# Kernel optimization log

Hardware: AMD Instinct MI355X
Metric: run time of the kernel (lower is better)

## Reference

```python
import jax, jax.numpy as jnp
import numpy as np

K = 16            # neighbors per node
NB = 8            # number_of_basis
MAX_RADIUS = 10.0
MUL_1E = 32       # multiplicity of the 1e output block
DIM_0E = 64       # 64x0e block (structurally zero: no 1o x 0e -> 0e path)
DIM_2E = 80       # 16x2e block (structurally zero: no 1o x 0e -> 2e path)


def knn_edges(coords):
    """coords [B,N,3] -> (senders, receivers) flat int32 indices of length B*N*K.
    Edge (j -> i): j is one of the K nearest neighbors of i (self excluded),
    matching torch_geometric knn_graph(loop=False, flow=source_to_target)."""
    B, N, _ = coords.shape
    n2 = jnp.sum(coords * coords, -1)                       # [B,N]
    d2 = n2[:, :, None] + n2[:, None, :] - 2.0 * jnp.einsum('bnd,bmd->bnm', coords, coords)
    d2 = d2 + jnp.eye(N, dtype=coords.dtype) * 1e10         # exclude self-loops
    _, idx = jax.lax.top_k(-d2, K)                          # [B,N,K] neighbor ids per node
    offs = (jnp.arange(B) * N)[:, None, None]
    senders = (idx + offs).reshape(-1)
    receivers = (jnp.broadcast_to(jnp.arange(N)[None, :, None], (B, N, K)) + offs).reshape(-1)
    return senders, receivers


def gaussian_soft_one_hot(x, number):
    # x in [0,1], shape [E,1] -> [E,number]
    centers = jnp.linspace(0.0, 1.0, number).astype(x.dtype)
    sigma = 1.0 / number
    g = jnp.exp(-(x - centers) ** 2 / (2.0 * sigma * sigma))
    s = jnp.sum(g, -1, keepdims=True)
    s = jnp.where(s > 0, s, jnp.ones_like(s))
    return g / s


def setup_inputs():
    key = jax.random.key(0)
    ks = jax.random.split(key, 6)
    B, N = 8, 4096
    coords = jax.random.normal(ks[0], (B, N, 3), dtype=jnp.float32) * 10.0
    atom_types = jax.random.randint(ks[1], (B, N), 0, 20)
    residue_types = jax.random.randint(ks[2], (B, N), 0, 21)
    tp_weight = jax.random.normal(ks[3], (NB, MUL_1E), dtype=jnp.float32) / np.sqrt(NB)
    atom_emb = jax.random.normal(ks[4], (20, 112), dtype=jnp.float32).at[0].set(0.0)   # padding_idx=0
    res_emb = jax.random.normal(ks[5], (21, 112), dtype=jnp.float32).at[0].set(0.0)    # padding_idx=0
    return {"coords": coords, "atom_types": atom_types, "residue_types": residue_types,
            "tp_weight": tp_weight, "atom_emb": atom_emb, "res_emb": res_emb}


def reference(coords, atom_types, residue_types, tp_weight, atom_emb, res_emb):
    B, N, _ = coords.shape
    E = B * N * K
    senders, receivers = knn_edges(coords)
    cf = coords.reshape(-1, 3)
    r = cf[senders] - cf[receivers]                           # [E,3]
    dist = jnp.linalg.norm(r, axis=-1, keepdims=True)         # [E,1]
    r_hat = r / (dist + 1e-8)
    cutoff = jnp.clip(dist / MAX_RADIUS, 0.0, 1.0)
    rb = gaussian_soft_one_hot(cutoff, NB)                    # [E,NB]
    # FullyConnectedTensorProduct(1x1o/1e, NBx0e -> ... 32x1e ...):
    feat_1e = jnp.einsum('ev,vw,em->ewm', rb, tp_weight, r_hat) / np.sqrt(3.0)  # [E,32,3]
    # scatter_mean over receivers
    num = jax.ops.segment_sum(feat_1e.reshape(E, MUL_1E * 3), receivers, num_segments=B * N)
    cnt = jax.ops.segment_sum(jnp.ones((E,), coords.dtype), receivers, num_segments=B * N)
    agg_1e = (num / jnp.maximum(cnt, 1.0)[:, None]).reshape(B, N, MUL_1E * 3)
    zeros0 = jnp.zeros((B, N, DIM_0E), coords.dtype)
    zeros2 = jnp.zeros((B, N, DIM_2E), coords.dtype)
    pos_feats = jnp.concatenate([zeros0, agg_1e, zeros2], -1)  # [B,N,240]
    node_features = jnp.concatenate([pos_feats, atom_emb[atom_types], res_emb[residue_types]], -1)
    return node_features  # [B,N,464]
```

## Files before the change

### kernel.cpp

```cpp
#include <hip/hip_runtime.h>
#include <hip/hip_bf16.h>

#define NN    4096
#define KNEI  16
#define QPW   4
#define WPB   16
#define BLOCK (WPB * 64)
#define QPB   (WPB * QPW)
#define NEGB  -3.0e38f
#define PACKM 0xFFFFFFC0

typedef float f32x2 __attribute__((ext_vector_type(2)));

__device__ __forceinline__ int rlane(int v, int l)
{ return __builtin_amdgcn_readlane(v, l); }
__device__ __forceinline__ float rlanef(float v, int l)
{ return __int_as_float(__builtin_amdgcn_readlane(__float_as_int(v), l)); }

template<int CTRL>
__device__ __forceinline__ void amax_step(float& f, int& i)
{
    int fs = __builtin_amdgcn_update_dpp(__float_as_int(f), __float_as_int(f),
                                         CTRL, 0xF, 0xF, false);
    int is = __builtin_amdgcn_update_dpp(i, i, CTRL, 0xF, 0xF, false);
    float ff = __int_as_float(fs);
    bool gt = ff > f;
    f = gt ? ff : f;
    i = gt ? is : i;
}

__device__ __forceinline__ void wave_amax(float f, int i, float& M, int& mi)
{
    amax_step<0x111>(f, i); amax_step<0x112>(f, i); amax_step<0x114>(f, i);
    amax_step<0x118>(f, i); amax_step<0x142>(f, i); amax_step<0x143>(f, i);
    M  = rlanef(f, 63);
    mi = rlane(i, 63);
}

__device__ __forceinline__ void row_amax(float& f, int& i)
{
    amax_step<0x121>(f, i); amax_step<0x122>(f, i);
    amax_step<0x124>(f, i); amax_step<0x128>(f, i);
}

__device__ __forceinline__ float row16_sum_dpp(float v)
{
    float f = v;
#define STEPA(CTRL)                                                          \
    { int s_ = __builtin_amdgcn_update_dpp(0, __float_as_int(f),             \
               (CTRL), 0xF, 0xF, true);                                      \
      f += __int_as_float(s_); }
    STEPA(0x111) STEPA(0x112) STEPA(0x114) STEPA(0x118)
#undef STEPA
    return f;
}

__device__ __forceinline__ float bpermf(int abyte, float v)
{ return __int_as_float(__builtin_amdgcn_ds_bpermute(abyte, __float_as_int(v))); }

__device__ __forceinline__ float sel4f(float a, float b, float c, float d, int q)
{
    float lo = (q & 1) ? b : a;
    float hi = (q & 1) ? d : c;
    return (q & 2) ? hi : lo;
}

#define LADDER(dp, b, s)                                          \
    {  (s) = __builtin_amdgcn_fmed3f((dp), (s), (b));             \
       (b) = fmaxf((b), (dp)); }

#define SELFFIX(q, b, s)                                                     \
    {  int cb_ = __float_as_int(b) & 63;                                     \
       if ((((cb_) << 6) | (lane ^ cb_)) == q0 + (q)) { (b) = (s); (s) = NEGB; } \
       int cs_ = __float_as_int(s) & 63;                                     \
       if ((((cs_) << 6) | (lane ^ cs_)) == q0 + (q)) { (s) = NEGB; } }

#define REPLAY(q, xq, yq, zq)                                                \
    {   int colq = rlane(colw, 16 * (q));                                    \
        int kq   = rlane(kw,   16 * (q));                                    \
        int j2 = (lane << 6) | (colq ^ lane);                                \
        float4 P = pts[j2];                                                  \
        float scr = fmaf(P.x, (xq), fmaf(P.y, (yq), fmaf(P.z, (zq), P.w)));  \
        float sf = __int_as_float((__float_as_int(scr) & PACKM) | lane);     \
        if (j2 == q0 + (q)) sf = NEGB;                                       \
        _Pragma("unroll")                                                    \
        for (int t = 0; t < KNEI; ++t) {                                     \
            int sv = rlane(selIdx, 16 * (q) + t);                            \
            if (j2 == sv) sf = NEGB;                                         \
        }                                                                    \
        float M1; int i1;                                                    \
        wave_amax(sf, j2, M1, i1);                                           \
        float sf2 = (j2 == i1) ? NEGB : sf;                                  \
        float M2; int i2;                                                    \
        wave_amax(sf2, j2, M2, i2);                                          \
        bool ow = (lane == 16 * (q) + (colq & 15));                          \
        if (kq == 0)      { pb0 = ow ? M1 : pb0; ps0 = ow ? M2 : ps0; }      \
        else if (kq == 1) { pb1 = ow ? M1 : pb1; ps1 = ow ? M2 : ps1; }      \
        else if (kq == 2) { pb2 = ow ? M1 : pb2; ps2 = ow ? M2 : ps2; }      \
        else              { pb3 = ow ? M1 : pb3; ps3 = ow ? M2 : ps3; }      \
    }

#define PROMOTE(k, pb, ps)                                                   \
    {   bool pk = own && (kw == (k));                                        \
        exh = exh || (pk && ((ps) == NEGB));                                 \
        (pb) = pk ? (ps)  : (pb);                                            \
        (ps) = pk ? NEGB : (ps);                                             \
    }

__global__ __launch_bounds__(BLOCK, 8)
void protein_enc_kernel(const float* __restrict__ coords,
                        const int*   __restrict__ atypes,
                        const int*   __restrict__ rtypes,
                        const float* __restrict__ tpw,
                        const float* __restrict__ aemb,
                        const float* __restrict__ remb,
                        float* __restrict__ out)
{
    __shared__ float4 pts[NN];
    __shared__ float  sW[8 * 32];

    const int tid  = threadIdx.x;
    const int lane = tid & 63;
    const int wv   = tid >> 6;
    const int bpb  = NN / QPB;
    const int batch    = blockIdx.x / bpb;
    const int nodeBase = (blockIdx.x % bpb) * QPB;

    const float* cb = coords + (size_t)batch * NN * 3;

    for (int p = tid; p < NN; p += BLOCK) {
        float x = cb[3*p], y = cb[3*p+1], z = cb[3*p+2];
        pts[p] = make_float4(x, y, z, -0.5f * (x*x + y*y + z*z));
    }
    if (tid < 256) sW[tid] = tpw[tid];
    __syncthreads();

    const int q0 = nodeBase + wv * QPW;
    const float4 P0 = pts[q0],   P1 = pts[q0+1];
    const float4 P2 = pts[q0+2], P3 = pts[q0+3];
    const float x0 = P0.x, y0 = P0.y, z0 = P0.z;
    const float x1 = P1.x, y1 = P1.y, z1 = P1.z;
    const float x2 = P2.x, y2 = P2.y, z2 = P2.z;
    const float x3 = P3.x, y3 = P3.y, z3 = P3.z;

    const f32x2 qAx = {x0, x1}, qAy = {y0, y1}, qAz = {z0, z1};
    const f32x2 qBx = {x2, x3}, qBy = {y2, y3}, qBz = {z2, z3};

    float b0 = NEGB, s0 = NEGB, b1 = NEGB, s1 = NEGB;
    float b2 = NEGB, s2 = NEGB, b3 = NEGB, s3 = NEGB;

    #pragma unroll 8
    for (int c = 0; c < NN / 64; ++c) {
        int j = (c << 6) | (lane ^ c);
        float4 P = pts[j];
        f32x2 Px = {P.x, P.x}, Py = {P.y, P.y}, Pz = {P.z, P.z}, Pw = {P.w, P.w};
        f32x2 dA = __builtin_elementwise_fma(Px, qAx,
                   __builtin_elementwise_fma(Py, qAy,
                   __builtin_elementwise_fma(Pz, qAz, Pw)));
        f32x2 dB = __builtin_elementwise_fma(Px, qBx,
                   __builtin_elementwise_fma(Py, qBy,
                   __builtin_elementwise_fma(Pz, qBz, Pw)));
        float d0 = __int_as_float((__float_as_int(dA.x) & PACKM) | c);
        float d1 = __int_as_float((__float_as_int(dA.y) & PACKM) | c);
        float d2 = __int_as_float((__float_as_int(dB.x) & PACKM) | c);
        float d3 = __int_as_float((__float_as_int(dB.y) & PACKM) | c);
        LADDER(d0, b0, s0)
        LADDER(d1, b1, s1)
        LADDER(d2, b2, s2)
        LADDER(d3, b3, s3)
    }

    SELFFIX(0, b0, s0)
    SELFFIX(1, b1, s1)
    SELFFIX(2, b2, s2)
    SELFFIX(3, b3, s3)

    const int q  = lane >> 4;
    const int gt = lane & 15;
    float pb0, pb1, pb2, pb3, ps0, ps1, ps2, ps3;
    {
        const int ab = gt << 2;
#define PULL(K, PB, PS)                                                      \
        {   int a = ab + ((K) << 6);                                         \
            PB = sel4f(bpermf(a,b0), bpermf(a,b1), bpermf(a,b2), bpermf(a,b3), q); \
            PS = sel4f(bpermf(a,s0), bpermf(a,s1), bpermf(a,s2), bpermf(a,s3), q); \
        }
        PULL(0, pb0, ps0)
        PULL(1, pb1, ps1)
        PULL(2, pb2, ps2)
        PULL(3, pb3, ps3)
#undef PULL
    }

    int selIdx = -1;

    #pragma unroll 1
    for (int r = 0; r < KNEI; ++r) {
        float f = fmaxf(fmaxf(pb0, pb1), fmaxf(pb2, pb3));
        int k = (f == pb3) ? 3 : ((f == pb2) ? 2 : ((f == pb1) ? 1 : 0));
        int cw = __float_as_int(f) & 63;
        int col = gt + (k << 4);
        int jl = (cw << 6) | (col ^ cw);
        int i = (k << 12) | jl;
        row_amax(f, i);

        int j  = i & 4095;
        int kw = i >> 12;
        int colw = (j & 63) ^ (j >> 6);
        bool own = (gt == (colw & 15));

        if (gt == r) selIdx = j;

        bool exh = false;
        PROMOTE(0, pb0, ps0)
        PROMOTE(1, pb1, ps1)
        PROMOTE(2, pb2, ps2)
        PROMOTE(3, pb3, ps3)

        unsigned long long ex = __ballot(exh);
        if (ex) {
            if ((ex >>  0) & 0xFFFFull) REPLAY(0, x0, y0, z0)
            if ((ex >> 16) & 0xFFFFull) REPLAY(1, x1, y1, z1)
            if ((ex >> 32) & 0xFFFFull) REPLAY(2, x2, y2, z2)
            if ((ex >> 48) & 0xFFFFull) REPLAY(3, x3, y3, z3)
        }
    }

    float xq = (q & 2) ? ((q & 1) ? x3 : x2) : ((q & 1) ? x1 : x0);
    float yq = (q & 2) ? ((q & 1) ? y3 : y2) : ((q & 1) ? y1 : y0);
    float zq = (q & 2) ? ((q & 1) ? z3 : z2) : ((q & 1) ? z1 : z0);

    float4 P = pts[selIdx];
    float rx = P.x - xq, ry = P.y - yq, rz = P.z - zq;
    float dist = sqrtf(rx*rx + ry*ry + rz*rz);
    float inv  = 1.0f / (dist + 1e-8f);
    float hx = rx * inv, hy = ry * inv, hz = rz * inv;
    float cu = fminf(dist / 10.0f, 1.0f);
    float gg[8], ssum = 0.0f;
    #pragma unroll
    for (int v = 0; v < 8; ++v) {
        float d = cu - (float)v * (1.0f / 7.0f);
        gg[v] = expf(d * d * -32.0f);
        ssum += gg[v];
    }
    float is = 1.0f / ssum;
    float S[24];
    #pragma unroll
    for (int v = 0; v < 8; ++v) {
        float rbv = gg[v] * is;
        S[3*v]   = rbv * hx;
        S[3*v+1] = rbv * hy;
        S[3*v+2] = rbv * hz;
    }
    #pragma unroll
    for (int t = 0; t < 24; ++t) S[t] = row16_sum_dpp(S[t]);

    float wcol[8];
    #pragma unroll
    for (int v = 0; v < 8; ++v) wcol[v] = sW[32*v + (lane & 31)];

    const float scale = 0.036084391824351613f;
    const float4 z4 = make_float4(0.f, 0.f, 0.f, 0.f);

    #pragma unroll
    for (int qq = 0; qq < QPW; ++qq) {
        const int gq = batch * NN + q0 + qq;
        float sg[24];
        #pragma unroll
        for (int t = 0; t < 24; ++t) sg[t] = rlanef(S[t], 16 * qq + 15);

        float* onode = out + (size_t)gq * 464;
        float4* o4 = (float4*)onode;
        if (lane < 16)       o4[lane] = z4;
        else if (lane < 36)  o4[lane + 24] = z4;

        if (lane < 32) {
            float a0 = 0.f, a1 = 0.f, a2 = 0.f;
            #pragma unroll
            for (int v = 0; v < 8; ++v) {
                a0 = fmaf(wcol[v], sg[3*v],   a0);
                a1 = fmaf(wcol[v], sg[3*v+1], a1);
                a2 = fmaf(wcol[v], sg[3*v+2], a2);
            }
            onode[64 + 3*lane]     = a0 * scale;
            onode[64 + 3*lane + 1] = a1 * scale;
            onode[64 + 3*lane + 2] = a2 * scale;
        }

        const int at = atypes[gq];
        const int rt = rtypes[gq];
        if (lane < 56) {
            float4 v = (lane < 28)
                ? ((const float4*)(aemb + 112*at))[lane]
                : ((const float4*)(remb + 112*rt))[lane - 28];
            o4[60 + lane] = v;
        }
    }
}

extern "C" void kernel_launch(void* const* d_in, const int* in_sizes, int n_in,
                              void* d_out, int out_size, void* d_ws, size_t ws_size,
                              hipStream_t stream)
{
    const float* coords = (const float*)d_in[0];
    const int*   at     = (const int*)  d_in[1];
    const int*   rt     = (const int*)  d_in[2];
    const float* tpw    = (const float*)d_in[3];
    const float* ae     = (const float*)d_in[4];
    const float* re     = (const float*)d_in[5];
    float* out = (float*)d_out;

    const int B = in_sizes[1] / NN;
    dim3 grid(B * (NN / QPB));
    protein_enc_kernel<<<grid, BLOCK, 0, stream>>>(coords, at, rt, tpw, ae, re, out);
}
```

Baseline: 73.80 us.

## Vectorize top-2 ladder, simplify k-select round, factor Gaussian exps

The main scan's top-2 ladder now runs on packed f32x2 vectors with max/min instead of per-query fmed3. The 16-round selection replaces the row argmax that carried indices with a float-only DPP max, followed by a ballot to pick the winning lane. Selected indices go to shared memory, so replay reads them with int4 loads instead of 16 readlanes. The 8 Gaussian basis exps become 2 exps plus a multiplicative recurrence with precomputed constants, which may cost some accuracy or risk underflow in the small terms.

```diff
diff --git a/kernel.cpp b/kernel.cpp
--- a/kernel.cpp
+++ b/kernel.cpp
@@ -11,11 +11,20 @@
 #define PACKM 0xFFFFFFC0
 
 typedef float f32x2 __attribute__((ext_vector_type(2)));
+typedef int   i32x2 __attribute__((ext_vector_type(2)));
 
 __device__ __forceinline__ int rlane(int v, int l)
 { return __builtin_amdgcn_readlane(v, l); }
 __device__ __forceinline__ float rlanef(float v, int l)
 { return __int_as_float(__builtin_amdgcn_readlane(__float_as_int(v), l)); }
+
+template<int CTRL>
+__device__ __forceinline__ float rmax_step(float f)
+{
+    int s_ = __builtin_amdgcn_update_dpp(__float_as_int(f), __float_as_int(f),
+                                         CTRL, 0xF, 0xF, false);
+    return fmaxf(f, __int_as_float(s_));
+}
 
 template<int CTRL>
 __device__ __forceinline__ void amax_step(float& f, int& i)
@@ -35,12 +44,6 @@
     amax_step<0x118>(f, i); amax_step<0x142>(f, i); amax_step<0x143>(f, i);
     M  = rlanef(f, 63);
     mi = rlane(i, 63);
-}
-
-__device__ __forceinline__ void row_amax(float& f, int& i)
-{
-    amax_step<0x121>(f, i); amax_step<0x122>(f, i);
-    amax_step<0x124>(f, i); amax_step<0x128>(f, i);
 }
 
 __device__ __forceinline__ float row16_sum_dpp(float v)
@@ -65,46 +68,37 @@
     return (q & 2) ? hi : lo;
 }
 
-#define LADDER(dp, b, s)                                          \
-    {  (s) = __builtin_amdgcn_fmed3f((dp), (s), (b));             \
-       (b) = fmaxf((b), (dp)); }
-
 #define SELFFIX(q, b, s)                                                     \
     {  int cb_ = __float_as_int(b) & 63;                                     \
        if ((((cb_) << 6) | (lane ^ cb_)) == q0 + (q)) { (b) = (s); (s) = NEGB; } \
        int cs_ = __float_as_int(s) & 63;                                     \
        if ((((cs_) << 6) | (lane ^ cs_)) == q0 + (q)) { (s) = NEGB; } }
 
-#define REPLAY(q, xq, yq, zq)                                                \
-    {   int colq = rlane(colw, 16 * (q));                                    \
-        int kq   = rlane(kw,   16 * (q));                                    \
+#define REPLAY(qq, xq, yq, zq)                                               \
+    {   int wq = __ffsll(ex & (0xFFFFull << ((qq) * 16))) - 1;               \
+        int colq = rlane(col, wq);                                           \
+        int kq   = rlane(kf,  wq);                                           \
         int j2 = (lane << 6) | (colq ^ lane);                                \
-        float4 P = pts[j2];                                                  \
-        float scr = fmaf(P.x, (xq), fmaf(P.y, (yq), fmaf(P.z, (zq), P.w)));  \
+        float4 Pp = pts[j2];                                                 \
+        float scr = fmaf(Pp.x,(xq), fmaf(Pp.y,(yq), fmaf(Pp.z,(zq), Pp.w))); \
         float sf = __int_as_float((__float_as_int(scr) & PACKM) | lane);     \
-        if (j2 == q0 + (q)) sf = NEGB;                                       \
-        _Pragma("unroll")                                                    \
-        for (int t = 0; t < KNEI; ++t) {                                     \
-            int sv = rlane(selIdx, 16 * (q) + t);                            \
-            if (j2 == sv) sf = NEGB;                                         \
-        }                                                                    \
+        if (j2 == q0 + (qq)) sf = NEGB;                                      \
+        const int4* sp = (const int4*)&sel[wv * 64 + ((qq) << 4)];           \
+        int4 sa = sp[0], sb = sp[1], sc = sp[2], sd = sp[3];                 \
+        if (j2==sa.x || j2==sa.y || j2==sa.z || j2==sa.w) sf = NEGB;         \
+        if (j2==sb.x || j2==sb.y || j2==sb.z || j2==sb.w) sf = NEGB;         \
+        if (j2==sc.x || j2==sc.y || j2==sc.z || j2==sc.w) sf = NEGB;         \
+        if (j2==sd.x || j2==sd.y || j2==sd.z || j2==sd.w) sf = NEGB;         \
         float M1; int i1;                                                    \
         wave_amax(sf, j2, M1, i1);                                           \
         float sf2 = (j2 == i1) ? NEGB : sf;                                  \
         float M2; int i2;                                                    \
         wave_amax(sf2, j2, M2, i2);                                          \
-        bool ow = (lane == 16 * (q) + (colq & 15));                          \
+        bool ow = (lane == (qq) * 16 + (colq & 15));                         \
         if (kq == 0)      { pb0 = ow ? M1 : pb0; ps0 = ow ? M2 : ps0; }      \
         else if (kq == 1) { pb1 = ow ? M1 : pb1; ps1 = ow ? M2 : ps1; }      \
         else if (kq == 2) { pb2 = ow ? M1 : pb2; ps2 = ow ? M2 : ps2; }      \
         else              { pb3 = ow ? M1 : pb3; ps3 = ow ? M2 : ps3; }      \
-    }
-
-#define PROMOTE(k, pb, ps)                                                   \
-    {   bool pk = own && (kw == (k));                                        \
-        exh = exh || (pk && ((ps) == NEGB));                                 \
-        (pb) = pk ? (ps)  : (pb);                                            \
-        (ps) = pk ? NEGB : (ps);                                             \
     }
 
 __global__ __launch_bounds__(BLOCK, 8)
@@ -118,6 +112,7 @@
 {
     __shared__ float4 pts[NN];
     __shared__ float  sW[8 * 32];
+    __shared__ int    sel[WPB * 64];
 
     const int tid  = threadIdx.x;
     const int lane = tid & 63;
@@ -133,6 +128,7 @@
         pts[p] = make_float4(x, y, z, -0.5f * (x*x + y*y + z*z));
     }
     if (tid < 256) sW[tid] = tpw[tid];
+    sel[wv * 64 + lane] = -1;
     __syncthreads();
 
     const int q0 = nodeBase + wv * QPW;
@@ -145,30 +141,35 @@
 
     const f32x2 qAx = {x0, x1}, qAy = {y0, y1}, qAz = {z0, z1};
     const f32x2 qBx = {x2, x3}, qBy = {y2, y3}, qBz = {z2, z3};
-
-    float b0 = NEGB, s0 = NEGB, b1 = NEGB, s1 = NEGB;
-    float b2 = NEGB, s2 = NEGB, b3 = NEGB, s3 = NEGB;
+    const i32x2 M2v = {(int)PACKM, (int)PACKM};
+
+    f32x2 bA = {NEGB, NEGB}, sA = {NEGB, NEGB};
+    f32x2 bB = {NEGB, NEGB}, sB = {NEGB, NEGB};
 
     #pragma unroll 8
     for (int c = 0; c < NN / 64; ++c) {
         int j = (c << 6) | (lane ^ c);
         float4 P = pts[j];
-        f32x2 Px = {P.x, P.x}, Py = {P.y, P.y}, Pz = {P.z, P.z}, Pw = {P.w, P.w};
-        f32x2 dA = __builtin_elementwise_fma(Px, qAx,
-                   __builtin_elementwise_fma(Py, qAy,
-                   __builtin_elementwise_fma(Pz, qAz, Pw)));
-        f32x2 dB = __builtin_elementwise_fma(Px, qBx,
-                   __builtin_elementwise_fma(Py, qBy,
-                   __builtin_elementwise_fma(Pz, qBz, Pw)));
-        float d0 = __int_as_float((__float_as_int(dA.x) & PACKM) | c);
-        float d1 = __int_as_float((__float_as_int(dA.y) & PACKM) | c);
-        float d2 = __int_as_float((__float_as_int(dB.x) & PACKM) | c);
-        float d3 = __int_as_float((__float_as_int(dB.y) & PACKM) | c);
-        LADDER(d0, b0, s0)
-        LADDER(d1, b1, s1)
-        LADDER(d2, b2, s2)
-        LADDER(d3, b3, s3)
-    }
+        f32x2 vx = {P.x, P.x}, vy = {P.y, P.y}, vz = {P.z, P.z}, vw = {P.w, P.w};
+        f32x2 dA = __builtin_elementwise_fma(vx, qAx,
+                   __builtin_elementwise_fma(vy, qAy,
+                   __builtin_elementwise_fma(vz, qAz, vw)));
+        f32x2 dB = __builtin_elementwise_fma(vx, qBx,
+                   __builtin_elementwise_fma(vy, qBy,
+                   __builtin_elementwise_fma(vz, qBz, vw)));
+        i32x2 cc = {c, c};
+        f32x2 pA = __builtin_bit_cast(f32x2,
+                     (__builtin_bit_cast(i32x2, dA) & M2v) | cc);
+        f32x2 pB = __builtin_bit_cast(f32x2,
+                     (__builtin_bit_cast(i32x2, dB) & M2v) | cc);
+        sA = __builtin_elementwise_max(sA, __builtin_elementwise_min(pA, bA));
+        bA = __builtin_elementwise_max(bA, pA);
+        sB = __builtin_elementwise_max(sB, __builtin_elementwise_min(pB, bB));
+        bB = __builtin_elementwise_max(bB, pB);
+    }
+
+    float b0 = bA.x, b1 = bA.y, b2 = bB.x, b3 = bB.y;
+    float s0 = sA.x, s1 = sA.y, s2 = sB.x, s3 = sB.y;
 
     SELFFIX(0, b0, s0)
     SELFFIX(1, b1, s1)
@@ -192,32 +193,34 @@
 #undef PULL
     }
 
-    int selIdx = -1;
+    const unsigned long long gmask = 0xFFFFull << (q << 4);
+    const int selbase = wv * 64 + (q << 4);
 
     #pragma unroll 1
     for (int r = 0; r < KNEI; ++r) {
         float f = fmaxf(fmaxf(pb0, pb1), fmaxf(pb2, pb3));
-        int k = (f == pb3) ? 3 : ((f == pb2) ? 2 : ((f == pb1) ? 1 : 0));
-        int cw = __float_as_int(f) & 63;
-        int col = gt + (k << 4);
-        int jl = (cw << 6) | (col ^ cw);
-        int i = (k << 12) | jl;
-        row_amax(f, i);
-
-        int j  = i & 4095;
-        int kw = i >> 12;
-        int colw = (j & 63) ^ (j >> 6);
-        bool own = (gt == (colw & 15));
-
-        if (gt == r) selIdx = j;
-
-        bool exh = false;
-        PROMOTE(0, pb0, ps0)
-        PROMOTE(1, pb1, ps1)
-        PROMOTE(2, pb2, ps2)
-        PROMOTE(3, pb3, ps3)
-
-        unsigned long long ex = __ballot(exh);
+        f = rmax_step<0x121>(f); f = rmax_step<0x122>(f);
+        f = rmax_step<0x124>(f); f = rmax_step<0x128>(f);
+        bool c0 = (pb0 == f), c1 = (pb1 == f), c2 = (pb2 == f), c3 = (pb3 == f);
+        unsigned long long m = __ballot(c0 | c1 | c2 | c3);
+        int w = __ffsll(m & gmask) - 1;
+        bool iwin = (lane == w);
+        int kf = c0 ? 0 : (c1 ? 1 : (c2 ? 2 : 3));
+        bool o0 = iwin && c0;
+        bool o1 = iwin && !c0 && c1;
+        bool o2 = iwin && !c0 && !c1 && c2;
+        bool o3 = iwin && !c0 && !c1 && !c2;
+        int cw  = __float_as_int(f) & 63;
+        int col = gt + (kf << 4);
+        int jw  = (cw << 6) | (col ^ cw);
+        if (iwin) sel[selbase + r] = jw;
+        float pskf = o1 ? ps1 : (o2 ? ps2 : (o3 ? ps3 : ps0));
+        bool e = iwin && (pskf == NEGB);
+        pb0 = o0 ? ps0 : pb0;  ps0 = o0 ? NEGB : ps0;
+        pb1 = o1 ? ps1 : pb1;  ps1 = o1 ? NEGB : ps1;
+        pb2 = o2 ? ps2 : pb2;  ps2 = o2 ? NEGB : ps2;
+        pb3 = o3 ? ps3 : pb3;  ps3 = o3 ? NEGB : ps3;
+        unsigned long long ex = __ballot(e);
         if (ex) {
             if ((ex >>  0) & 0xFFFFull) REPLAY(0, x0, y0, z0)
             if ((ex >> 16) & 0xFFFFull) REPLAY(1, x1, y1, z1)
@@ -226,6 +229,8 @@
         }
     }
 
+    int selIdx = sel[wv * 64 + lane];
+
     float xq = (q & 2) ? ((q & 1) ? x3 : x2) : ((q & 1) ? x1 : x0);
     float yq = (q & 2) ? ((q & 1) ? y3 : y2) : ((q & 1) ? y1 : y0);
     float zq = (q & 2) ? ((q & 1) ? z3 : z2) : ((q & 1) ? z1 : z0);
@@ -236,13 +241,16 @@
     float inv  = 1.0f / (dist + 1e-8f);
     float hx = rx * inv, hy = ry * inv, hz = rz * inv;
     float cu = fminf(dist / 10.0f, 1.0f);
-    float gg[8], ssum = 0.0f;
-    #pragma unroll
-    for (int v = 0; v < 8; ++v) {
-        float d = cu - (float)v * (1.0f / 7.0f);
-        gg[v] = expf(d * d * -32.0f);
-        ssum += gg[v];
-    }
+    float A = expf(cu * cu * -32.0f);
+    float E = expf(cu * (64.0f / 7.0f));
+    const float K[8] = {1.0f, 0.5204501f, 0.0733697f, 0.00280164f,
+                        2.897772e-05f, 8.11857e-08f, 6.16130e-11f,
+                        1.2664166e-14f};
+    float gg[8];
+    float t = A, ssum = A;
+    gg[0] = A;
+    #pragma unroll
+    for (int v = 1; v < 8; ++v) { t *= E; gg[v] = t * K[v]; ssum += gg[v]; }
     float is = 1.0f / ssum;
     float S[24];
     #pragma unroll
@@ -253,7 +261,7 @@
         S[3*v+2] = rbv * hz;
     }
     #pragma unroll
-    for (int t = 0; t < 24; ++t) S[t] = row16_sum_dpp(S[t]);
+    for (int t2 = 0; t2 < 24; ++t2) S[t2] = row16_sum_dpp(S[t2]);
 
     float wcol[8];
     #pragma unroll
@@ -267,7 +275,7 @@
         const int gq = batch * NN + q0 + qq;
         float sg[24];
         #pragma unroll
-        for (int t = 0; t < 24; ++t) sg[t] = rlanef(S[t], 16 * qq + 15);
+        for (int t2 = 0; t2 < 24; ++t2) sg[t2] = rlanef(S[t2], 16 * qq + 15);
 
         float* onode = out + (size_t)gq * 464;
         float4* o4 = (float4*)onode;
```

After: 73.71 us. About the same (-0.1%).
